# Kernel tuning notes

Hardware: AMD Instinct MI355X
Metric: run time of the kernel (lower is better)

The kernel has to match this reference:

```python
import jax, jax.numpy as jnp
import numpy as np

B, IN, H, OUT, E = 16384, 256, 512, 32, 8

def setup_inputs() -> dict:
    key = jax.random.key(0)
    ks = jax.random.split(key, 4)
    s1 = 1.0 / np.sqrt(IN); s2 = 1.0 / np.sqrt(H); s3 = 1.0 / np.sqrt(H)
    return {
        "inputs": jax.random.normal(ks[0], (B, IN), dtype=jnp.float32),
        "W1": jax.random.normal(ks[1], (E, IN, H), dtype=jnp.float32) * s1,
        "b1": jnp.zeros((E, H), dtype=jnp.float32),
        "W2": jax.random.normal(ks[2], (E, H, H), dtype=jnp.float32) * s2,
        "b2": jnp.zeros((E, H), dtype=jnp.float32),
        "W3": jax.random.normal(ks[3], (E, H, OUT), dtype=jnp.float32) * s3,
        "b3": jnp.zeros((E, OUT), dtype=jnp.float32),
    }

def reference(inputs, W1, b1, W2, b2, W3, b3):
    # Batched over ensemble dim e: each member is Dense(relu)->Dense(relu)->Dense(linear).
    # inputs: [B, IN]; W1: [E, IN, H]; output: [B, E, OUT] (matches tf.stack(output, axis=1)).
    h = jax.nn.relu(jnp.einsum('bi,eih->beh', inputs, W1) + b1[None, :, :])
    h = jax.nn.relu(jnp.einsum('beh,ehk->bek', h, W2) + b2[None, :, :])
    out = jnp.einsum('beh,eho->beo', h, W3) + b3[None, :, :]
    return out
```

## Files before the change

### kernel.cpp

```cpp
#include <hip/hip_runtime.h>
#include <stdint.h>

typedef short bf16x8 __attribute__((ext_vector_type(8)));
typedef float f32x4  __attribute__((ext_vector_type(4)));

__device__ __forceinline__ uint16_t f2bf(float f) {
    uint32_t u = __float_as_uint(f);
    u += 0x7FFF + ((u >> 16) & 1);
    return (uint16_t)(u >> 16);
}
__device__ __forceinline__ uint32_t pk2bf(float a, float b) {
    return (uint32_t)f2bf(a) | ((uint32_t)f2bf(b) << 16);
}

typedef __attribute__((address_space(1))) const uint32_t gu32;
typedef __attribute__((address_space(3))) uint32_t lu32;
__device__ __forceinline__ void gload16(const void* g, void* l) {
    __builtin_amdgcn_global_load_lds((gu32*)g, (lu32*)l, 16, 0, 0);
}

__global__ __launch_bounds__(256) void prep(
    const float* __restrict__ X,  const float* __restrict__ W1,
    const float* __restrict__ W2, const float* __restrict__ W3,
    uint16_t* __restrict__ xbf, uint16_t* __restrict__ w1t,
    uint16_t* __restrict__ w2t, uint16_t* __restrict__ w3t)
{
    const int b = blockIdx.x, tid = threadIdx.x;
    if (b < 4096) {
        const int i = b * 256 + tid;
        const float4 v = ((const float4*)X)[i];
        ushort4 h;
        h.x = f2bf(v.x); h.y = f2bf(v.y); h.z = f2bf(v.z); h.w = f2bf(v.w);
        ((ushort4*)xbf)[i] = h;
        return;
    }
    __shared__ float t[32][33];
    const int tx = tid & 31, ty = tid >> 5;
    const float* in; uint16_t* out; int R, C, bx, by, e;
    if (b < 5120) {
        const int bb = b - 4096; e = bb >> 7; const int rem = bb & 127;
        bx = rem & 15; by = rem >> 4; R = 256; C = 512; in = W1; out = w1t;
    } else if (b < 7168) {
        const int bb = b - 5120; e = bb >> 8; const int rem = bb & 255;
        bx = rem & 15; by = rem >> 4; R = 512; C = 512; in = W2; out = w2t;
    } else {
        const int bb = b - 7168; e = bb >> 4; bx = 0; by = bb & 15;
        R = 512; C = 32; in = W3; out = w3t;
    }
    const int r0 = by * 32, c0 = bx * 32;
    const float* ine = in + (size_t)e * R * C;
    uint16_t* oute   = out + (size_t)e * R * C;
#pragma unroll
    for (int j = 0; j < 4; ++j)
        t[ty + 8 * j][tx] = ine[(size_t)(r0 + ty + 8 * j) * C + (c0 + tx)];
    __syncthreads();
#pragma unroll
    for (int j = 0; j < 4; ++j) {
        const int orow = c0 + ty + 8 * j;
        const int ocol = r0 + tx;
        oute[(size_t)orow * R + ocol] = f2bf(t[tx][ty + 8 * j]);
    }
}

__global__ __launch_bounds__(512, 1) void fused128c(
    const uint16_t* __restrict__ xbf,
    const uint16_t* __restrict__ W1t, const float* __restrict__ b1,
    const uint16_t* __restrict__ W2t, const float* __restrict__ b2,
    const uint16_t* __restrict__ W3t, const float* __restrict__ b3,
    float* __restrict__ out)
{
    extern __shared__ char smem[];
    char* h1buf = smem;
    char* wstg  = smem + 131072;

    const int tid = threadIdx.x, wid = tid >> 6, lane = tid & 63;
    const int kg = lane >> 4, lr = lane & 15;
    const int e   = blockIdx.x;
    const int bm0 = blockIdx.y * 128;
    const int wm = wid >> 2, wn = wid & 3;
    const int rlo = lane >> 3, pslot = lane & 7;
    const int lswz = (pslot ^ rlo) * 8;

    const uint16_t* Xb  = xbf + (size_t)bm0 * 256;
    const uint16_t* W1e = W1t + (size_t)e * 512 * 256;
    const uint16_t* W2e = W2t + (size_t)e * 512 * 512;
    const uint16_t* W3e = W3t + (size_t)e * 32 * 512;

    auto stageW = [&](const uint16_t* We, int K, int cur, int nq, int kt) {
#pragma unroll
        for (int i = 0; i < 2; ++i) {
            const int r = wid * 16 + i * 8 + rlo;
            gload16(We + (size_t)(nq * 128 + r) * K + kt * 64 + lswz,
                    wstg + cur * 16384 + r * 128 + lane * 16);
        }
    };

#pragma unroll
    for (int kt = 0; kt < 4; ++kt)
#pragma unroll
        for (int i = 0; i < 2; ++i) {
            const int rb = wid * 16 + i * 8;
            gload16(Xb + (size_t)(rb + rlo) * 256 + kt * 64 + lswz,
                    h1buf + kt * 16384 + rb * 128 + lane * 16);
        }
    stageW(W1e, 256, 0, 0, 0);
    __syncthreads();

    f32x4 a1[4][4][2];
#pragma unroll
    for (int q = 0; q < 4; ++q)
#pragma unroll
        for (int b = 0; b < 4; ++b)
#pragma unroll
            for (int c = 0; c < 2; ++c) a1[q][b][c] = f32x4{0.f, 0.f, 0.f, 0.f};

#pragma unroll
    for (int p = 0; p < 16; ++p) {
        const int nq = p >> 2, kt = p & 3, cur = p & 1;
        if (p + 1 < 16) stageW(W1e, 256, cur ^ 1, (p + 1) >> 2, (p + 1) & 3);
        asm volatile("" ::: "memory");
        __builtin_amdgcn_s_setprio(1);
#pragma unroll
        for (int kh = 0; kh < 2; ++kh) {
            bf16x8 wf[2], af[4];
#pragma unroll
            for (int c = 0; c < 2; ++c) {
                const int row = wn * 32 + c * 16 + lr;
                wf[c] = *(const bf16x8*)(wstg + cur * 16384 + row * 128 +
                                         (((kh * 4 + kg) ^ (row & 7)) << 4));
            }
#pragma unroll
            for (int b = 0; b < 4; ++b) {
                const int row = wm * 64 + b * 16 + lr;
                af[b] = *(const bf16x8*)(h1buf + kt * 16384 + row * 128 +
                                         (((kh * 4 + kg) ^ (row & 7)) << 4));
            }
#pragma unroll
            for (int b = 0; b < 4; ++b)
#pragma unroll
                for (int c = 0; c < 2; ++c)
                    a1[nq][b][c] = __builtin_amdgcn_mfma_f32_16x16x32_bf16(wf[c], af[b], a1[nq][b][c], 0, 0, 0);
        }
        __builtin_amdgcn_s_setprio(0);
        __syncthreads();
    }

#pragma unroll
    for (int nq = 0; nq < 4; ++nq)
#pragma unroll
        for (int c = 0; c < 2; ++c) {
            const int col = nq * 128 + wn * 32 + c * 16 + kg * 4;
            const float4 bv = *(const float4*)(b1 + e * 512 + col);
#pragma unroll
            for (int b = 0; b < 4; ++b) {
                const float x0 = fmaxf(a1[nq][b][c][0] + bv.x, 0.f);
                const float x1 = fmaxf(a1[nq][b][c][1] + bv.y, 0.f);
                const float x2 = fmaxf(a1[nq][b][c][2] + bv.z, 0.f);
                const float x3 = fmaxf(a1[nq][b][c][3] + bv.w, 0.f);
                uint2 w;
                w.x = pk2bf(x0, x1);
                w.y = pk2bf(x2, x3);
                const int row = wm * 64 + b * 16 + lr;
                *(uint2*)(h1buf + row * 1024 + (((col << 1)) ^ ((row & 7) << 5))) = w;
            }
        }
    __syncthreads();

    const int mf = wid >> 1, of = wid & 1;
    f32x4 o3[2];
    o3[0] = f32x4{0.f, 0.f, 0.f, 0.f};
    o3[1] = f32x4{0.f, 0.f, 0.f, 0.f};

#pragma unroll
    for (int nq = 0; nq < 4; ++nq) {
        stageW(W2e, 512, 0, nq, 0);
        __syncthreads();

        f32x4 a2[4][2];
#pragma unroll
        for (int b = 0; b < 4; ++b)
#pragma unroll
            for (int c = 0; c < 2; ++c) a2[b][c] = f32x4{0.f, 0.f, 0.f, 0.f};

#pragma unroll
        for (int kt = 0; kt < 8; ++kt) {
            const int cur = kt & 1;
            if (kt + 1 < 8) stageW(W2e, 512, cur ^ 1, nq, kt + 1);
            asm volatile("" ::: "memory");
            __builtin_amdgcn_s_setprio(1);
#pragma unroll
            for (int kh = 0; kh < 2; ++kh) {
                bf16x8 wf[2], af[4];
#pragma unroll
                for (int c = 0; c < 2; ++c) {
                    const int row = wn * 32 + c * 16 + lr;
                    wf[c] = *(const bf16x8*)(wstg + cur * 16384 + row * 128 +
                                             (((kh * 4 + kg) ^ (row & 7)) << 4));
                }
                const int kbyte = kt * 128 + kh * 64 + kg * 16;
#pragma unroll
                for (int b = 0; b < 4; ++b) {
                    const int row = wm * 64 + b * 16 + lr;
                    af[b] = *(const bf16x8*)(h1buf + row * 1024 +
                                             (kbyte ^ ((row & 7) << 5)));
                }
#pragma unroll
                for (int b = 0; b < 4; ++b)
#pragma unroll
                    for (int c = 0; c < 2; ++c)
                        a2[b][c] = __builtin_amdgcn_mfma_f32_16x16x32_bf16(wf[c], af[b], a2[b][c], 0, 0, 0);
            }
            __builtin_amdgcn_s_setprio(0);
            __syncthreads();
        }

#pragma unroll
        for (int c = 0; c < 2; ++c) {
            const int colh = wn * 32 + c * 16 + kg * 4;
            const float4 bv = *(const float4*)(b2 + e * 512 + nq * 128 + colh);
#pragma unroll
            for (int b = 0; b < 4; ++b) {
                const float x0 = fmaxf(a2[b][c][0] + bv.x, 0.f);
                const float x1 = fmaxf(a2[b][c][1] + bv.y, 0.f);
                const float x2 = fmaxf(a2[b][c][2] + bv.z, 0.f);
                const float x3 = fmaxf(a2[b][c][3] + bv.w, 0.f);
                uint2 w;
                w.x = pk2bf(x0, x1);
                w.y = pk2bf(x2, x3);
                const int row = wm * 64 + b * 16 + lr;
                *(uint2*)(wstg + row * 256 + (((colh << 1)) ^ ((row & 7) << 5))) = w;
            }
        }
        __syncthreads();

#pragma unroll
        for (int kcq = 0; kcq < 4; ++kcq)
#pragma unroll
            for (int b2f = 0; b2f < 2; ++b2f) {
                const int row = mf * 32 + b2f * 16 + lr;
                const bf16x8 hb = *(const bf16x8*)(wstg + row * 256 +
                                                   ((kcq * 64 + kg * 16) ^ ((row & 7) << 5)));
                const bf16x8 w3 = *(const bf16x8*)(W3e + (size_t)(of * 16 + lr) * 512 +
                                                   nq * 128 + kcq * 32 + kg * 8);
                o3[b2f] = __builtin_amdgcn_mfma_f32_16x16x32_bf16(w3, hb, o3[b2f], 0, 0, 0);
            }
        __syncthreads();
    }

#pragma unroll
    for (int b2f = 0; b2f < 2; ++b2f) {
        const int col = e * 32 + of * 16 + kg * 4;
        const float4 bv = *(const float4*)(b3 + col);
        const int row = bm0 + mf * 32 + b2f * 16 + lr;
        float4 res;
        res.x = o3[b2f][0] + bv.x;
        res.y = o3[b2f][1] + bv.y;
        res.z = o3[b2f][2] + bv.z;
        res.w = o3[b2f][3] + bv.w;
        *(float4*)(out + (size_t)row * 256 + col) = res;
    }
}

extern "C" void kernel_launch(void* const* d_in, const int* in_sizes, int n_in,
                              void* d_out, int out_size, void* d_ws, size_t ws_size,
                              hipStream_t stream) {
    (void)in_sizes; (void)n_in; (void)out_size; (void)ws_size;
    const float* X  = (const float*)d_in[0];
    const float* W1 = (const float*)d_in[1];
    const float* b1 = (const float*)d_in[2];
    const float* W2 = (const float*)d_in[3];
    const float* b2 = (const float*)d_in[4];
    const float* W3 = (const float*)d_in[5];
    const float* b3 = (const float*)d_in[6];
    float* out = (float*)d_out;

    uint16_t* w1t = (uint16_t*)d_ws;
    uint16_t* w2t = w1t + 8 * 256 * 512;
    uint16_t* w3t = w2t + 8 * 512 * 512;
    uint16_t* xbf = w3t + 8 * 512 * 32;

    prep<<<7296, 256, 0, stream>>>(X, W1, W2, W3, xbf, w1t, w2t, w3t);

    (void)hipFuncSetAttribute((const void*)fused128c,
                              hipFuncAttributeMaxDynamicSharedMemorySize, 163840);
    fused128c<<<dim3(8, 128), 512, 163840, stream>>>(xbf, w1t, b1, w2t, b2,
                                                     w3t, b3, out);
}
```

Baseline: 142.8 us.

## Widen layer-1 weight tiles to 256 columns and prefetch first W2 tile early

Layer 1 now processes the 512 hidden outputs in two halves of 256 columns instead of four quarters of 128. Each weight tile is staged in the unused upper part of the h1 buffer, and each wave computes a 64x64 sub-tile. This halves the number of stage/sync iterations and raises the MFMA-per-LDS-read ratio. The first W2 tile load is also issued before the layer-1 epilogue so its latency overlaps the bias/ReLU/bf16 writes, dropping one barrier. The cost is higher accumulator register pressure (32 f32x4 per wave is unchanged but with 4 wide B fragments) and a dependence on h1buf regions not overlapping the layer-1 weight staging.

```diff
diff --git a/kernel.cpp b/kernel.cpp
--- a/kernel.cpp
+++ b/kernel.cpp
@@ -62,7 +62,7 @@
     }
 }
 
-__global__ __launch_bounds__(512, 1) void fused128c(
+__global__ __launch_bounds__(512, 1) void fused128d(
     const uint16_t* __restrict__ xbf,
     const uint16_t* __restrict__ W1t, const float* __restrict__ b1,
     const uint16_t* __restrict__ W2t, const float* __restrict__ b2,
@@ -86,12 +86,20 @@
     const uint16_t* W2e = W2t + (size_t)e * 512 * 512;
     const uint16_t* W3e = W3t + (size_t)e * 32 * 512;
 
-    auto stageW = [&](const uint16_t* We, int K, int cur, int nq, int kt) {
+    auto stageW1 = [&](int s, int nh, int kt) {
+#pragma unroll
+        for (int g = 0; g < 4; ++g) {
+            const int rb = g * 64 + wid * 8;
+            gload16(W1e + (size_t)(nh * 256 + rb + rlo) * 256 + kt * 64 + lswz,
+                    h1buf + 65536 + s * 32768 + rb * 128 + lane * 16);
+        }
+    };
+    auto stageW2 = [&](int cur, int nq, int kt) {
 #pragma unroll
         for (int i = 0; i < 2; ++i) {
-            const int r = wid * 16 + i * 8 + rlo;
-            gload16(We + (size_t)(nq * 128 + r) * K + kt * 64 + lswz,
-                    wstg + cur * 16384 + r * 128 + lane * 16);
+            const int rb = wid * 16 + i * 8;
+            gload16(W2e + (size_t)(nq * 128 + rb + rlo) * 512 + kt * 64 + lswz,
+                    wstg + cur * 16384 + rb * 128 + lane * 16);
         }
     };
 
@@ -103,30 +111,31 @@
             gload16(Xb + (size_t)(rb + rlo) * 256 + kt * 64 + lswz,
                     h1buf + kt * 16384 + rb * 128 + lane * 16);
         }
-    stageW(W1e, 256, 0, 0, 0);
+    stageW1(0, 0, 0);
     __syncthreads();
 
-    f32x4 a1[4][4][2];
-#pragma unroll
-    for (int q = 0; q < 4; ++q)
+    f32x4 a1[2][4][4];
+#pragma unroll
+    for (int q = 0; q < 2; ++q)
 #pragma unroll
         for (int b = 0; b < 4; ++b)
 #pragma unroll
-            for (int c = 0; c < 2; ++c) a1[q][b][c] = f32x4{0.f, 0.f, 0.f, 0.f};
-
-#pragma unroll
-    for (int p = 0; p < 16; ++p) {
-        const int nq = p >> 2, kt = p & 3, cur = p & 1;
-        if (p + 1 < 16) stageW(W1e, 256, cur ^ 1, (p + 1) >> 2, (p + 1) & 3);
+            for (int c = 0; c < 4; ++c) a1[q][b][c] = f32x4{0.f, 0.f, 0.f, 0.f};
+
+#pragma unroll
+    for (int p = 0; p < 8; ++p) {
+        const int nh = p >> 2, kt = p & 3, cur = p & 1;
+        if (p + 1 < 8) stageW1(cur ^ 1, (p + 1) >> 2, (p + 1) & 3);
         asm volatile("" ::: "memory");
+        const char* sW = h1buf + 65536 + cur * 32768;
         __builtin_amdgcn_s_setprio(1);
 #pragma unroll
         for (int kh = 0; kh < 2; ++kh) {
-            bf16x8 wf[2], af[4];
-#pragma unroll
-            for (int c = 0; c < 2; ++c) {
-                const int row = wn * 32 + c * 16 + lr;
-                wf[c] = *(const bf16x8*)(wstg + cur * 16384 + row * 128 +
+            bf16x8 wf[4], af[4];
+#pragma unroll
+            for (int c = 0; c < 4; ++c) {
+                const int row = wn * 64 + c * 16 + lr;
+                wf[c] = *(const bf16x8*)(sW + row * 128 +
                                          (((kh * 4 + kg) ^ (row & 7)) << 4));
             }
 #pragma unroll
@@ -138,25 +147,27 @@
 #pragma unroll
             for (int b = 0; b < 4; ++b)
 #pragma unroll
-                for (int c = 0; c < 2; ++c)
-                    a1[nq][b][c] = __builtin_amdgcn_mfma_f32_16x16x32_bf16(wf[c], af[b], a1[nq][b][c], 0, 0, 0);
+                for (int c = 0; c < 4; ++c)
+                    a1[nh][b][c] = __builtin_amdgcn_mfma_f32_16x16x32_bf16(wf[c], af[b], a1[nh][b][c], 0, 0, 0);
         }
         __builtin_amdgcn_s_setprio(0);
         __syncthreads();
     }
 
-#pragma unroll
-    for (int nq = 0; nq < 4; ++nq)
-#pragma unroll
-        for (int c = 0; c < 2; ++c) {
-            const int col = nq * 128 + wn * 32 + c * 16 + kg * 4;
+    stageW2(0, 0, 0);
+
+#pragma unroll
+    for (int nh = 0; nh < 2; ++nh)
+#pragma unroll
+        for (int c = 0; c < 4; ++c) {
+            const int col = nh * 256 + wn * 64 + c * 16 + kg * 4;
             const float4 bv = *(const float4*)(b1 + e * 512 + col);
 #pragma unroll
             for (int b = 0; b < 4; ++b) {
-                const float x0 = fmaxf(a1[nq][b][c][0] + bv.x, 0.f);
-                const float x1 = fmaxf(a1[nq][b][c][1] + bv.y, 0.f);
-                const float x2 = fmaxf(a1[nq][b][c][2] + bv.z, 0.f);
-                const float x3 = fmaxf(a1[nq][b][c][3] + bv.w, 0.f);
+                const float x0 = fmaxf(a1[nh][b][c][0] + bv.x, 0.f);
+                const float x1 = fmaxf(a1[nh][b][c][1] + bv.y, 0.f);
+                const float x2 = fmaxf(a1[nh][b][c][2] + bv.z, 0.f);
+                const float x3 = fmaxf(a1[nh][b][c][3] + bv.w, 0.f);
                 uint2 w;
                 w.x = pk2bf(x0, x1);
                 w.y = pk2bf(x2, x3);
@@ -173,8 +184,10 @@
 
 #pragma unroll
     for (int nq = 0; nq < 4; ++nq) {
-        stageW(W2e, 512, 0, nq, 0);
-        __syncthreads();
+        if (nq > 0) {
+            stageW2(0, nq, 0);
+            __syncthreads();
+        }
 
         f32x4 a2[4][2];
 #pragma unroll
@@ -185,7 +198,7 @@
 #pragma unroll
         for (int kt = 0; kt < 8; ++kt) {
             const int cur = kt & 1;
-            if (kt + 1 < 8) stageW(W2e, 512, cur ^ 1, nq, kt + 1);
+            if (kt + 1 < 8) stageW2(cur ^ 1, nq, kt + 1);
             asm volatile("" ::: "memory");
             __builtin_amdgcn_s_setprio(1);
 #pragma unroll
@@ -281,8 +294,8 @@
 
     prep<<<7296, 256, 0, stream>>>(X, W1, W2, W3, xbf, w1t, w2t, w3t);
 
-    (void)hipFuncSetAttribute((const void*)fused128c,
+    (void)hipFuncSetAttribute((const void*)fused128d,
                               hipFuncAttributeMaxDynamicSharedMemorySize, 163840);
-    fused128c<<<dim3(8, 128), 512, 163840, stream>>>(xbf, w1t, b1, w2t, b2,
+    fused128d<<<dim3(8, 128), 512, 163840, stream>>>(xbf, w1t, b1, w2t, b2,
                                                      w3t, b3, out);
 }
```

New measurement: 139.5 us. 2.3% less time.
